# Performance work log

Hardware: AMD Instinct MI355X
Metric: run time of the kernel (lower is better)

Reference implementation:

```python
import jax, jax.numpy as jnp
import numpy as np

TEMPERATURE = 0.07
EPS = 1e-06


def setup_inputs() -> dict:
    key = jax.random.key(0)
    k1, k2 = jax.random.split(key)
    feats = jax.random.normal(k1, (8192, 512), dtype=jnp.float32)
    # module expects L2-normalized features
    feats = feats / jnp.linalg.norm(feats, axis=1, keepdims=True)
    labels = jax.random.randint(k2, (8192,), 0, 100, dtype=jnp.int64 if jax.config.jax_enable_x64 else jnp.int32)
    return {"features": feats, "labels": labels}


def reference(features, labels):
    n = features.shape[0]
    sim = jnp.matmul(features, features.T)                      # [N, N]
    lab = labels.reshape(-1, 1)
    mask = (lab == lab.T).astype(features.dtype)                # same-class mask
    logits_mask = 1.0 - jnp.eye(n, dtype=features.dtype)        # exclude self
    mask = mask * logits_mask
    logits = sim / TEMPERATURE
    logits_max = jax.lax.stop_gradient(jnp.max(logits, axis=1, keepdims=True))
    logits = logits - logits_max
    exp_logits = jnp.exp(logits) * logits_mask
    log_prob = logits - jnp.log(jnp.sum(exp_logits, axis=1, keepdims=True) + EPS)
    mean_log_prob_pos = jnp.sum(mask * log_prob, axis=1) / (jnp.sum(mask, axis=1) + EPS)
    return -jnp.mean(mean_log_prob_pos)
```

## Files before the change

kernel.cpp:

```cpp
#include <hip/hip_runtime.h>

#define NN 8192
#define KK 512
#define INVT 14.285714285714286f
#define K2E 20.60992915555662f
#define EPSF 1e-6f

#define NB 64
#define NTRI (NB * (NB + 1) / 2)

typedef short bf16x8 __attribute__((ext_vector_type(8)));
typedef float f32x4 __attribute__((ext_vector_type(4)));

__device__ __forceinline__ unsigned short f2bf(float f) {
  unsigned int u = __float_as_uint(f);
  u = u + 0x7FFFu + ((u >> 16) & 1u);
  return (unsigned short)(u >> 16);
}

__device__ __forceinline__ void load_lds16(const void* g, void* l) {
  __builtin_amdgcn_global_load_lds(
      (const __attribute__((address_space(1))) unsigned int*)g,
      (__attribute__((address_space(3))) unsigned int*)l, 16, 0, 0);
}

__global__ void prep_kernel(const float* __restrict__ feats,
                            const int* __restrict__ labels,
                            unsigned short* __restrict__ fb,
                            int* __restrict__ cnt) {
  int tid = blockIdx.x * 256 + threadIdx.x;
  const float4* src = (const float4*)feats + (size_t)tid * 2;
  float4 a = src[0];
  float4 b = src[1];
  bf16x8 o;
  o[0] = (short)f2bf(a.x); o[1] = (short)f2bf(a.y);
  o[2] = (short)f2bf(a.z); o[3] = (short)f2bf(a.w);
  o[4] = (short)f2bf(b.x); o[5] = (short)f2bf(b.y);
  o[6] = (short)f2bf(b.z); o[7] = (short)f2bf(b.w);
  *(bf16x8*)(fb + (size_t)tid * 8) = o;
  if (tid < NN) atomicAdd(&cnt[labels[tid]], 1);
}

__global__ __launch_bounds__(256, 2) void
scl_main_kernel(const unsigned short* __restrict__ fb,
                const int* __restrict__ labels,
                float* __restrict__ Sarr, float* __restrict__ Parr) {
  __shared__ unsigned short lds[64 * KK];

  int rb = 0, rem = blockIdx.x;
  while (rem >= NB - rb) { rem -= NB - rb; ++rb; }
  const int cb = rb + rem;
  const bool diag = (rb == cb);

  const int tid = threadIdx.x;
  const int w = tid >> 6;
  const int l = tid & 63;
  const int lo = l & 15;
  const int g = l >> 4;

  const int row0 = rb * 128 + w * 32;
  const int colBase = cb * 128;
  const int myrow0 = row0 + g * 4;
  const int myrow1 = row0 + 16 + g * 4;

  bf16x8 Af0[16], Af1[16];
  {
    const unsigned short* a0 = fb + (size_t)(row0 + lo) * KK;
    const unsigned short* a1 = fb + (size_t)(row0 + 16 + lo) * KK;
#pragma unroll
    for (int ks = 0; ks < 16; ++ks) {
      Af0[ks] = *(const bf16x8*)(a0 + ks * 32 + g * 8);
      Af1[ks] = *(const bf16x8*)(a1 + ks * 32 + g * 8);
    }
  }

  int labr0[4], labr1[4];
#pragma unroll
  for (int r = 0; r < 4; ++r) {
    labr0[r] = labels[myrow0 + r];
    labr1[r] = labels[myrow1 + r];
  }
  int labc[2][4];
#pragma unroll
  for (int h = 0; h < 2; ++h)
#pragma unroll
    for (int st = 0; st < 4; ++st)
      labc[h][st] = labels[colBase + h * 64 + st * 16 + lo];

  f32x4 Sac0 = {0.f,0.f,0.f,0.f}, Sac1 = {0.f,0.f,0.f,0.f};
  f32x4 Pac0 = {0.f,0.f,0.f,0.f}, Pac1 = {0.f,0.f,0.f,0.f};

#pragma unroll
  for (int h = 0; h < 2; ++h) {
    const int colb = colBase + h * 64;
    __syncthreads();
#pragma unroll
    for (int j = 0; j < 16; ++j) {
      const int col = w * 16 + j;
      const int kc = (l & 56) | ((l ^ col) & 7);
      const unsigned short* src = fb + (size_t)(colb + col) * KK + kc * 8;
      load_lds16((const void*)src, (void*)&lds[col * KK]);
    }
    __syncthreads();

#pragma unroll
    for (int st = 0; st < 4; ++st) {
      const int ct = st * 16 + lo;
      const int colg = colb + ct;
      const int lc = labc[h][st];
      f32x4 a0 = {0.f,0.f,0.f,0.f};
      f32x4 a1 = {0.f,0.f,0.f,0.f};
#pragma unroll
      for (int ks = 0; ks < 16; ++ks) {
        const int kc = ks * 4 + g;
        const int phys = (kc & 56) | ((kc ^ ct) & 7);
        bf16x8 Bf = *(const bf16x8*)(&lds[ct * KK + phys * 8]);
        a0 = __builtin_amdgcn_mfma_f32_16x16x32_bf16(Af0[ks], Bf, a0, 0, 0, 0);
        a1 = __builtin_amdgcn_mfma_f32_16x16x32_bf16(Af1[ks], Bf, a1, 0, 0, 0);
      }
      float ce = 0.f, cp = 0.f;
#pragma unroll
      for (int r = 0; r < 4; ++r) {
        const float s0 = a0[r];
        const float e0 = __builtin_amdgcn_exp2f(__builtin_fmaf(s0, K2E, -K2E));
        Sac0[r] += e0;
        ce += e0;
        if (lc == labr0[r]) { Pac0[r] += s0; cp += s0; }
        const float s1 = a1[r];
        const float e1 = __builtin_amdgcn_exp2f(__builtin_fmaf(s1, K2E, -K2E));
        Sac1[r] += e1;
        ce += e1;
        if (lc == labr1[r]) { Pac1[r] += s1; cp += s1; }
        if (diag) {
          if (colg == myrow0 + r) { Sac0[r] -= e0; Pac0[r] -= s0; }
          if (colg == myrow1 + r) { Sac1[r] -= e1; Pac1[r] -= s1; }
        }
      }
      if (!diag) {
        ce += __shfl_xor(ce, 16, 64);
        ce += __shfl_xor(ce, 32, 64);
        cp += __shfl_xor(cp, 16, 64);
        cp += __shfl_xor(cp, 32, 64);
        if (l < 16) {
          atomicAdd(&Sarr[colg], ce);
          atomicAdd(&Parr[colg], cp);
        }
      }
    }
  }

#pragma unroll
  for (int r = 0; r < 4; ++r) {
    float s0 = Sac0[r], p0 = Pac0[r], s1 = Sac1[r], p1 = Pac1[r];
#pragma unroll
    for (int m = 1; m < 16; m <<= 1) {
      s0 += __shfl_xor(s0, m, 64);
      p0 += __shfl_xor(p0, m, 64);
      s1 += __shfl_xor(s1, m, 64);
      p1 += __shfl_xor(p1, m, 64);
    }
    if (lo == 0) {
      atomicAdd(&Sarr[myrow0 + r], s0);
      atomicAdd(&Parr[myrow0 + r], p0);
      atomicAdd(&Sarr[myrow1 + r], s1);
      atomicAdd(&Parr[myrow1 + r], p1);
    }
  }
}

__global__ void finish_kernel(const float* __restrict__ Sarr,
                              const float* __restrict__ Parr,
                              const int* __restrict__ labels,
                              const int* __restrict__ cnt,
                              float* __restrict__ out) {
  int i = blockIdx.x * 256 + threadIdx.x;
  float v = 0.f;
  if (i < NN) {
    float C = (float)(cnt[labels[i]] - 1);
    float lp = Parr[i] * INVT - C * (INVT + logf(Sarr[i] + EPSF));
    v = lp / (C + EPSF);
  }
#pragma unroll
  for (int m = 1; m < 64; m <<= 1) v += __shfl_xor(v, m, 64);
  if ((threadIdx.x & 63) == 0) atomicAdd(out, -v * (1.0f / NN));
}

extern "C" void kernel_launch(void* const* d_in, const int* in_sizes, int n_in,
                              void* d_out, int out_size, void* d_ws, size_t ws_size,
                              hipStream_t stream) {
  const float* feats = (const float*)d_in[0];
  const int* labels = (const int*)d_in[1];

  unsigned short* fb = (unsigned short*)d_ws;
  const size_t FB_BYTES = (size_t)NN * KK * 2;
  float* Sarr = (float*)((char*)d_ws + FB_BYTES);
  float* Parr = Sarr + NN;
  int* cnt = (int*)(Parr + NN);

  hipMemsetAsync((char*)d_ws + FB_BYTES, 0, (size_t)NN * 8 + 512, stream);
  hipMemsetAsync(d_out, 0, sizeof(float), stream);

  prep_kernel<<<dim3((NN * KK / 8) / 256), dim3(256), 0, stream>>>(feats, labels, fb, cnt);
  scl_main_kernel<<<dim3(NTRI), dim3(256), 0, stream>>>(fb, labels, Sarr, Parr);
  finish_kernel<<<dim3(NN / 256), dim3(256), 0, stream>>>(Sarr, Parr, labels, cnt, (float*)d_out);
}
```

Before: 121.2 us.

## Replace global atomics with per-tile-block partial sums reduced in finish kernel

Row and column partial sums from each triangular tile are written to distinct slots in a [NB][N] partials buffer instead of atomically added to global arrays. Column contributions are first reduced across the four waves in LDS, so each block does plain stores. The finish kernel now sums the 64 partials per row, and the zeroing memset of the accumulators is dropped. This trades atomic contention for extra workspace traffic of several megabytes and a longer finish kernel.

```diff
diff --git a/kernel.cpp b/kernel.cpp
--- a/kernel.cpp
+++ b/kernel.cpp
@@ -44,7 +44,7 @@
 __global__ __launch_bounds__(256, 2) void
 scl_main_kernel(const unsigned short* __restrict__ fb,
                 const int* __restrict__ labels,
-                float* __restrict__ Sarr, float* __restrict__ Parr) {
+                float* __restrict__ Spart, float* __restrict__ Ppart) {
   __shared__ unsigned short lds[64 * KK];
 
   int rb = 0, rem = blockIdx.x;
@@ -89,6 +89,8 @@
 
   f32x4 Sac0 = {0.f,0.f,0.f,0.f}, Sac1 = {0.f,0.f,0.f,0.f};
   f32x4 Pac0 = {0.f,0.f,0.f,0.f}, Pac1 = {0.f,0.f,0.f,0.f};
+  float ceA[2][4] = {{0.f,0.f,0.f,0.f},{0.f,0.f,0.f,0.f}};
+  float cpA[2][4] = {{0.f,0.f,0.f,0.f},{0.f,0.f,0.f,0.f}};
 
 #pragma unroll
   for (int h = 0; h < 2; ++h) {
@@ -118,68 +120,92 @@
         a0 = __builtin_amdgcn_mfma_f32_16x16x32_bf16(Af0[ks], Bf, a0, 0, 0, 0);
         a1 = __builtin_amdgcn_mfma_f32_16x16x32_bf16(Af1[ks], Bf, a1, 0, 0, 0);
       }
-      float ce = 0.f, cp = 0.f;
 #pragma unroll
       for (int r = 0; r < 4; ++r) {
         const float s0 = a0[r];
         const float e0 = __builtin_amdgcn_exp2f(__builtin_fmaf(s0, K2E, -K2E));
         Sac0[r] += e0;
-        ce += e0;
-        if (lc == labr0[r]) { Pac0[r] += s0; cp += s0; }
+        ceA[h][st] += e0;
+        if (lc == labr0[r]) { Pac0[r] += s0; cpA[h][st] += s0; }
         const float s1 = a1[r];
         const float e1 = __builtin_amdgcn_exp2f(__builtin_fmaf(s1, K2E, -K2E));
         Sac1[r] += e1;
-        ce += e1;
-        if (lc == labr1[r]) { Pac1[r] += s1; cp += s1; }
+        ceA[h][st] += e1;
+        if (lc == labr1[r]) { Pac1[r] += s1; cpA[h][st] += s1; }
         if (diag) {
           if (colg == myrow0 + r) { Sac0[r] -= e0; Pac0[r] -= s0; }
           if (colg == myrow1 + r) { Sac1[r] -= e1; Pac1[r] -= s1; }
         }
       }
-      if (!diag) {
+    }
+  }
+
+#pragma unroll
+  for (int r = 0; r < 4; ++r) {
+    float s0 = Sac0[r], p0 = Pac0[r], s1 = Sac1[r], p1 = Pac1[r];
+#pragma unroll
+    for (int m = 1; m < 16; m <<= 1) {
+      s0 += __shfl_xor(s0, m, 64);
+      p0 += __shfl_xor(p0, m, 64);
+      s1 += __shfl_xor(s1, m, 64);
+      p1 += __shfl_xor(p1, m, 64);
+    }
+    if (lo == 0) {
+      Spart[cb * NN + myrow0 + r] = s0;
+      Ppart[cb * NN + myrow0 + r] = p0;
+      Spart[cb * NN + myrow1 + r] = s1;
+      Ppart[cb * NN + myrow1 + r] = p1;
+    }
+  }
+
+  if (!diag) {
+    __syncthreads();
+    float* redS = (float*)lds;
+    float* redP = redS + 512;
+#pragma unroll
+    for (int h = 0; h < 2; ++h) {
+#pragma unroll
+      for (int st = 0; st < 4; ++st) {
+        float ce = ceA[h][st], cp = cpA[h][st];
         ce += __shfl_xor(ce, 16, 64);
         ce += __shfl_xor(ce, 32, 64);
         cp += __shfl_xor(cp, 16, 64);
         cp += __shfl_xor(cp, 32, 64);
         if (l < 16) {
-          atomicAdd(&Sarr[colg], ce);
-          atomicAdd(&Parr[colg], cp);
+          redS[(w * 8 + h * 4 + st) * 16 + lo] = ce;
+          redP[(w * 8 + h * 4 + st) * 16 + lo] = cp;
         }
       }
     }
-  }
-
-#pragma unroll
-  for (int r = 0; r < 4; ++r) {
-    float s0 = Sac0[r], p0 = Pac0[r], s1 = Sac1[r], p1 = Pac1[r];
-#pragma unroll
-    for (int m = 1; m < 16; m <<= 1) {
-      s0 += __shfl_xor(s0, m, 64);
-      p0 += __shfl_xor(p0, m, 64);
-      s1 += __shfl_xor(s1, m, 64);
-      p1 += __shfl_xor(p1, m, 64);
-    }
-    if (lo == 0) {
-      atomicAdd(&Sarr[myrow0 + r], s0);
-      atomicAdd(&Parr[myrow0 + r], p0);
-      atomicAdd(&Sarr[myrow1 + r], s1);
-      atomicAdd(&Parr[myrow1 + r], p1);
-    }
-  }
-}
-
-__global__ void finish_kernel(const float* __restrict__ Sarr,
-                              const float* __restrict__ Parr,
+    __syncthreads();
+    if (tid < 128) {
+      const int slot = tid >> 4, ln = tid & 15;
+      float S = redS[slot * 16 + ln] + redS[(8 + slot) * 16 + ln] +
+                redS[(16 + slot) * 16 + ln] + redS[(24 + slot) * 16 + ln];
+      float P = redP[slot * 16 + ln] + redP[(8 + slot) * 16 + ln] +
+                redP[(16 + slot) * 16 + ln] + redP[(24 + slot) * 16 + ln];
+      const int colg = colBase + (slot >> 2) * 64 + (slot & 3) * 16 + ln;
+      Spart[rb * NN + colg] = S;
+      Ppart[rb * NN + colg] = P;
+    }
+  }
+}
+
+__global__ void finish_kernel(const float* __restrict__ Spart,
+                              const float* __restrict__ Ppart,
                               const int* __restrict__ labels,
                               const int* __restrict__ cnt,
                               float* __restrict__ out) {
   int i = blockIdx.x * 256 + threadIdx.x;
-  float v = 0.f;
-  if (i < NN) {
-    float C = (float)(cnt[labels[i]] - 1);
-    float lp = Parr[i] * INVT - C * (INVT + logf(Sarr[i] + EPSF));
-    v = lp / (C + EPSF);
-  }
+  float S = 0.f, P = 0.f;
+#pragma unroll 8
+  for (int p = 0; p < NB; ++p) {
+    S += Spart[p * NN + i];
+    P += Ppart[p * NN + i];
+  }
+  float C = (float)(cnt[labels[i]] - 1);
+  float lp = P * INVT - C * (INVT + logf(S + EPSF));
+  float v = lp / (C + EPSF);
 #pragma unroll
   for (int m = 1; m < 64; m <<= 1) v += __shfl_xor(v, m, 64);
   if ((threadIdx.x & 63) == 0) atomicAdd(out, -v * (1.0f / NN));
@@ -193,14 +219,14 @@
 
   unsigned short* fb = (unsigned short*)d_ws;
   const size_t FB_BYTES = (size_t)NN * KK * 2;
-  float* Sarr = (float*)((char*)d_ws + FB_BYTES);
-  float* Parr = Sarr + NN;
-  int* cnt = (int*)(Parr + NN);
-
-  hipMemsetAsync((char*)d_ws + FB_BYTES, 0, (size_t)NN * 8 + 512, stream);
+  float* Spart = (float*)((char*)d_ws + FB_BYTES);
+  float* Ppart = Spart + (size_t)NB * NN;
+  int* cnt = (int*)(Ppart + (size_t)NB * NN);
+
+  hipMemsetAsync(cnt, 0, 512, stream);
   hipMemsetAsync(d_out, 0, sizeof(float), stream);
 
   prep_kernel<<<dim3((NN * KK / 8) / 256), dim3(256), 0, stream>>>(feats, labels, fb, cnt);
-  scl_main_kernel<<<dim3(NTRI), dim3(256), 0, stream>>>(fb, labels, Sarr, Parr);
-  finish_kernel<<<dim3(NN / 256), dim3(256), 0, stream>>>(Sarr, Parr, labels, cnt, (float*)d_out);
-}
+  scl_main_kernel<<<dim3(NTRI), dim3(256), 0, stream>>>(fb, labels, Spart, Ppart);
+  finish_kernel<<<dim3(NN / 256), dim3(256), 0, stream>>>(Spart, Ppart, labels, cnt, (float*)d_out);
+}
```

After: 134.0 us. 1.11x slower.
